# Performance work log

Measured on AMD Instinct MI355X. Metric: run time of the kernel, lower is better.

## Reference

```python
import jax, jax.numpy as jnp
import numpy as np

B, S, D = 4, 2048, 1024
E = 8            # num_experts
F = 4096         # expert hidden dim (4*D)
T = B * S        # tokens
CAP = 1280       # capacity = ceil(1.25 * T / E)


def setup_inputs() -> dict:
    key = jax.random.key(0)
    k1, k2, k3, k4 = jax.random.split(key, 4)
    inputs = jax.random.normal(k1, (B, S, D), dtype=jnp.float32)
    gate_w = jax.random.normal(k2, (D, E), dtype=jnp.float32) / np.sqrt(D)
    w1 = jax.random.normal(k3, (E, D, F), dtype=jnp.float32) / np.sqrt(D)
    w2 = jax.random.normal(k4, (E, F, D), dtype=jnp.float32) / np.sqrt(F)
    return {"inputs": inputs, "gate_w": gate_w, "w1": w1, "w2": w2}


def reference(inputs, gate_w, w1, w2):
    tokens = inputs.reshape(-1, D)                       # [T, D]
    logits = tokens @ gate_w                             # [T, E] (gate, no bias)
    probs = jax.nn.softmax(logits, axis=-1)
    expert_idx = jnp.argmax(probs, axis=-1)              # top-1 routing
    mask1 = jax.nn.one_hot(expert_idx, E, dtype=tokens.dtype)        # [T, E]
    # position of each token within its chosen expert's queue
    pos = (jnp.cumsum(mask1, axis=0) - 1.0).astype(jnp.int32)        # [T, E]
    # one_hot of out-of-range (>= CAP) positions is all-zero -> capacity drop
    sec_mask = mask1[:, :, None] * jax.nn.one_hot(pos, CAP, dtype=tokens.dtype)  # [T, E, C]
    combine_weights = probs[:, :, None] * sec_mask       # [T, E, C]
    # dispatch: matmul(sec_mask.permute(1,2,0), tokens) -> [E, C, D]
    expert_input = jnp.einsum('tec,td->ecd', sec_mask, tokens)
    # grouped per-expert FFN
    h = jax.nn.relu(jnp.einsum('ecd,edf->ecf', expert_input, w1))    # [E, C, F]
    expert_output = jnp.einsum('ecf,efd->ecd', h, w2)                # [E, C, D]
    # combine: [T, E*C] @ [E*C, D]
    out = jnp.einsum('tec,ecd->td', combine_weights, expert_output)  # [T, D]
    return out.reshape(inputs.shape)
```

## Files before the change

### kernel.cpp

```cpp
#include <hip/hip_runtime.h>
#include <hip/hip_bf16.h>

#define TOKENS   8192
#define DDIM     1024
#define NEXP     8
#define FDIM     4096
#define CAPACITY 1280
#define NYT      10

typedef __attribute__((ext_vector_type(8))) __bf16 bf16x8;
typedef __attribute__((ext_vector_type(4))) __bf16 bf16x4;
typedef __attribute__((ext_vector_type(4))) float  f32x4;

typedef __attribute__((address_space(1))) const void gvoid_t;
typedef __attribute__((address_space(3))) void       lvoid_t;

__device__ __forceinline__ void async16(const void* g, void* l) {
  __builtin_amdgcn_global_load_lds((gvoid_t*)g, (lvoid_t*)l, 16, 0, 0);
}

__global__ void gate_kernel(const float* __restrict__ x, const float* __restrict__ gw,
                            int* __restrict__ eidx, float* __restrict__ prob) {
  const int t = blockIdx.x;
  const int lane = threadIdx.x;
  const float* xp = x + (size_t)t * DDIM;
  float acc[NEXP];
#pragma unroll
  for (int e = 0; e < NEXP; ++e) acc[e] = 0.f;
#pragma unroll 4
  for (int i = 0; i < DDIM / 64; ++i) {
    const int d = i * 64 + lane;
    const float xv = xp[d];
    const f32x4 g0 = *(const f32x4*)(gw + d * NEXP);
    const f32x4 g1 = *(const f32x4*)(gw + d * NEXP + 4);
    acc[0] += xv * g0[0]; acc[1] += xv * g0[1];
    acc[2] += xv * g0[2]; acc[3] += xv * g0[3];
    acc[4] += xv * g1[0]; acc[5] += xv * g1[1];
    acc[6] += xv * g1[2]; acc[7] += xv * g1[3];
  }
#pragma unroll
  for (int e = 0; e < NEXP; ++e) {
    float v = acc[e];
#pragma unroll
    for (int off = 32; off; off >>= 1) v += __shfl_xor(v, off);
    acc[e] = v;
  }
  if (lane == 0) {
    float m = acc[0]; int mi = 0;
#pragma unroll
    for (int e = 1; e < NEXP; ++e) if (acc[e] > m) { m = acc[e]; mi = e; }
    float s = 0.f;
#pragma unroll
    for (int e = 0; e < NEXP; ++e) s += __expf(acc[e] - m);
    eidx[t] = mi;
    prob[t] = 1.f / s;
  }
}

__global__ void scan_kernel(const int* __restrict__ eidx, int* __restrict__ src,
                            int* __restrict__ counts) {
  __shared__ int buf[2][NEXP][256];
  const int tid = threadIdx.x;
  for (int i = tid; i < NEXP * CAPACITY; i += 256) src[i] = -1;
  const int t0 = tid * (TOKENS / 256);
#pragma unroll
  for (int e = 0; e < NEXP; ++e) buf[0][e][tid] = 0;
  for (int k = 0; k < TOKENS / 256; ++k) {
    const int e = eidx[t0 + k];
    buf[0][e][tid]++;
  }
  __syncthreads();
  int cur = 0;
  for (int off = 1; off < 256; off <<= 1) {
#pragma unroll
    for (int e = 0; e < NEXP; ++e) {
      int v = buf[cur][e][tid];
      if (tid >= off) v += buf[cur][e][tid - off];
      buf[cur ^ 1][e][tid] = v;
    }
    __syncthreads();
    cur ^= 1;
  }
  if (tid < NEXP) counts[tid] = buf[cur][tid][255];
#pragma unroll
  for (int e = 0; e < NEXP; ++e)
    buf[cur ^ 1][e][tid] = (tid > 0) ? buf[cur][e][tid - 1] : 0;
  for (int k = 0; k < TOKENS / 256; ++k) {
    const int t = t0 + k;
    const int e = eidx[t];
    const int p = buf[cur ^ 1][e][tid]++;
    if (p < CAPACITY) src[e * CAPACITY + p] = t;
  }
}

__global__ void dispatch_kernel(const float* __restrict__ tokens, const int* __restrict__ src,
                                __bf16* __restrict__ Xb) {
  const int slot = blockIdx.x;
  const int tid  = threadIdx.x;
  const int t = src[slot];
  bf16x4* dst = (bf16x4*)(Xb + (size_t)slot * DDIM);
  bf16x4 o;
  if (t >= 0) {
    const f32x4 v = ((const f32x4*)(tokens + (size_t)t * DDIM))[tid];
    o[0] = (__bf16)v[0]; o[1] = (__bf16)v[1]; o[2] = (__bf16)v[2]; o[3] = (__bf16)v[3];
  } else {
    o[0] = (__bf16)0.f; o[1] = (__bf16)0.f; o[2] = (__bf16)0.f; o[3] = (__bf16)0.f;
  }
  dst[tid] = o;
}

__global__ void transpose_convert_kernel(const float* __restrict__ w, __bf16* __restrict__ wt,
                                         int R, int C) {
  __shared__ __bf16 tile[64][65];
  const int e = blockIdx.z;
  const float* wp = w + (size_t)e * R * C;
  __bf16* op = wt + (size_t)e * R * C;
  const int c0 = blockIdx.x * 64, r0 = blockIdx.y * 64;
  const int tx = threadIdx.x, ty = threadIdx.y;
#pragma unroll
  for (int i = 0; i < 16; ++i) {
    const int r = ty + i * 4;
    tile[r][tx] = (__bf16)wp[(size_t)(r0 + r) * C + c0 + tx];
  }
  __syncthreads();
#pragma unroll
  for (int i = 0; i < 16; ++i) {
    const int cc = ty + i * 4;
    op[(size_t)(c0 + cc) * R + r0 + tx] = tile[tx][cc];
  }
}

template <int MODE>
__global__ __launch_bounds__(256, 2)
void gemm_kernel(const __bf16* __restrict__ A, const __bf16* __restrict__ B,
                 __bf16* __restrict__ Cbf, float* __restrict__ out,
                 const int* __restrict__ src, const float* __restrict__ prob,
                 const int* __restrict__ counts,
                 int K, size_t sA, size_t sB, size_t sC) {
  constexpr int N  = (MODE == 0) ? FDIM : DDIM;
  constexpr int NX = N / 128;
  __shared__ char lds[2][32768];

  const int nwg = NX * NYT * NEXP;
  int wg = blockIdx.x;
  wg = (wg & 7) * (nwg >> 3) + (wg >> 3);
  const int e   = wg / (NX * NYT);
  const int rem = wg - e * (NX * NYT);
  const int ty  = rem % NYT;
  const int tx  = rem / NYT;
  const int m0  = ty * 128, n0 = tx * 128;

  const int cnt   = counts[e];
  const int tiles = (cnt + 127) >> 7;
  if (ty >= ((tiles < NYT) ? tiles : NYT)) return;

  const __bf16* Ae = A + (size_t)e * sA;
  const __bf16* Be = B + (size_t)e * sB;
  const int tid = threadIdx.x;
  const int wid = tid >> 6, lane = tid & 63;
  const int wm = wid >> 1, wn = wid & 1;
  const int rl = lane & 15, gl = lane >> 4;
  const int wu = __builtin_amdgcn_readfirstlane(tid) >> 6;

  f32x4 acc[4][4];
#pragma unroll
  for (int m = 0; m < 4; ++m)
#pragma unroll
    for (int n = 0; n < 4; ++n) acc[m][n] = (f32x4){0.f, 0.f, 0.f, 0.f};

  auto stage = [&](int c, int kt) {
    const int k0 = kt * 64;
#pragma unroll
    for (int i = 0; i < 4; ++i) {
      const int chunk = i * 4 + wu;
      const int s = chunk * 64 + lane;
      const int row = s >> 3, cg = (s & 7) ^ (row & 7);
      async16(Ae + (size_t)(m0 + row) * K + k0 + cg * 8, &lds[c][chunk * 1024]);
      async16(Be + (size_t)(n0 + row) * K + k0 + cg * 8, &lds[c][16384 + chunk * 1024]);
    }
  };

  auto phase = [&](int c, int kk) {
    bf16x8 af[4], bv[4];
#pragma unroll
    for (int m = 0; m < 4; ++m) {
      const int rowin = wm * 64 + m * 16 + rl;
      af[m] = *(const bf16x8*)(&lds[c][rowin * 128 + (((kk * 4 + gl) ^ (rowin & 7)) * 16)]);
    }
#pragma unroll
    for (int n = 0; n < 4; ++n) {
      const int rowin = wn * 64 + n * 16 + rl;
      bv[n] = *(const bf16x8*)(&lds[c][16384 + rowin * 128 +
                                       (((kk * 4 + gl) ^ (rowin & 7)) * 16)]);
    }
    __builtin_amdgcn_s_setprio(1);
#pragma unroll
    for (int m = 0; m < 4; ++m)
#pragma unroll
      for (int n = 0; n < 4; ++n)
        acc[m][n] = __builtin_amdgcn_mfma_f32_16x16x32_bf16(af[m], bv[n], acc[m][n], 0, 0, 0);
    __builtin_amdgcn_s_setprio(0);
  };

  const int nkt = K >> 6;
  stage(0, 0);
  __syncthreads();
  for (int t = 0; t < nkt; ++t) {
    const int cur = t & 1;
    if (t + 1 < nkt) stage(cur ^ 1, t + 1);
    phase(cur, 0);
    phase(cur, 1);
    if (t + 1 < nkt) __syncthreads();
  }

  if (MODE == 0) {
    __bf16* Ce = Cbf + (size_t)e * sC;
#pragma unroll
    for (int m = 0; m < 4; ++m)
#pragma unroll
      for (int j = 0; j < 4; ++j) {
        const int row = m0 + wm * 64 + m * 16 + gl * 4 + j;
#pragma unroll
        for (int n = 0; n < 4; ++n) {
          const int col = n0 + wn * 64 + n * 16 + rl;
          float v = acc[m][n][j];
          v = v > 0.f ? v : 0.f;
          Ce[(size_t)row * N + col] = (__bf16)v;
        }
      }
  } else {
#pragma unroll
    for (int m = 0; m < 4; ++m)
#pragma unroll
      for (int j = 0; j < 4; ++j) {
        const int slot = m0 + wm * 64 + m * 16 + gl * 4 + j;
        const int t = src[e * CAPACITY + slot];
        if (t >= 0) {
          const float p = prob[t];
          float* op = out + (size_t)t * N;
#pragma unroll
          for (int n = 0; n < 4; ++n) {
            const int col = n0 + wn * 64 + n * 16 + rl;
            op[col] = p * acc[m][n][j];
          }
        }
      }
  }
}

extern "C" void kernel_launch(void* const* d_in, const int* in_sizes, int n_in,
                              void* d_out, int out_size, void* d_ws, size_t ws_size,
                              hipStream_t stream) {
  const float* x  = (const float*)d_in[0];
  const float* gw = (const float*)d_in[1];
  const float* w1 = (const float*)d_in[2];
  const float* w2 = (const float*)d_in[3];
  float* out = (float*)d_out;

  char* ws = (char*)d_ws;
  size_t off = 0;
  auto alloc = [&](size_t bytes) {
    void* p = ws + off;
    off += (bytes + 255) & ~(size_t)255;
    return p;
  };
  __bf16* W1bT = (__bf16*)alloc((size_t)NEXP * FDIM * DDIM * 2);
  __bf16* W2bT = (__bf16*)alloc((size_t)NEXP * DDIM * FDIM * 2);
  __bf16* Xb   = (__bf16*)alloc((size_t)NEXP * CAPACITY * DDIM * 2);
  __bf16* Hb   = (__bf16*)alloc((size_t)NEXP * CAPACITY * FDIM * 2);
  int*   eidx  = (int*)alloc(TOKENS * sizeof(int));
  float* prob  = (float*)alloc(TOKENS * sizeof(float));
  int*   srcm  = (int*)alloc(NEXP * CAPACITY * sizeof(int));
  int*   cnts  = (int*)alloc(NEXP * sizeof(int));
  (void)ws_size; (void)in_sizes; (void)n_in;

  hipMemsetAsync(d_out, 0, (size_t)out_size * sizeof(float), stream);

  gate_kernel<<<TOKENS, 64, 0, stream>>>(x, gw, eidx, prob);
  scan_kernel<<<1, 256, 0, stream>>>(eidx, srcm, cnts);
  dispatch_kernel<<<NEXP * CAPACITY, 256, 0, stream>>>(x, srcm, Xb);
  transpose_convert_kernel<<<dim3(FDIM / 64, DDIM / 64, NEXP), dim3(64, 4), 0, stream>>>(
      w1, W1bT, DDIM, FDIM);
  transpose_convert_kernel<<<dim3(DDIM / 64, FDIM / 64, NEXP), dim3(64, 4), 0, stream>>>(
      w2, W2bT, FDIM, DDIM);
  gemm_kernel<0><<<(FDIM / 128) * NYT * NEXP, 256, 0, stream>>>(
      Xb, W1bT, Hb, nullptr, nullptr, nullptr, cnts,
      DDIM, (size_t)CAPACITY * DDIM, (size_t)FDIM * DDIM, (size_t)CAPACITY * FDIM);
  gemm_kernel<1><<<(DDIM / 128) * NYT * NEXP, 256, 0, stream>>>(
      Hb, W2bT, nullptr, out, srcm, prob, cnts,
      FDIM, (size_t)CAPACITY * FDIM, (size_t)DDIM * FDIM, 0);
}
```

Measured before the change: 366.9 us.

## Vectorize weight transpose and single-buffer the grouped GEMM LDS staging

The weight transpose-convert kernel now reads float4 vectors and writes 8-wide bf16 vectors through a padded tile, cutting scalar global memory transactions. The GEMM drops its double-buffered async prefetch and s_setprio hints in favour of a simple load, sync, compute, sync loop with half the LDS. The smaller LDS footprint may allow more resident workgroups, but global loads no longer overlap with MFMA work inside a workgroup.

```diff
diff --git a/kernel.cpp b/kernel.cpp
--- a/kernel.cpp
+++ b/kernel.cpp
@@ -111,22 +111,29 @@
 
 __global__ void transpose_convert_kernel(const float* __restrict__ w, __bf16* __restrict__ wt,
                                          int R, int C) {
-  __shared__ __bf16 tile[64][65];
+  __shared__ __bf16 tile[64][66];
   const int e = blockIdx.z;
   const float* wp = w + (size_t)e * R * C;
   __bf16* op = wt + (size_t)e * R * C;
   const int c0 = blockIdx.x * 64, r0 = blockIdx.y * 64;
-  const int tx = threadIdx.x, ty = threadIdx.y;
-#pragma unroll
-  for (int i = 0; i < 16; ++i) {
-    const int r = ty + i * 4;
-    tile[r][tx] = (__bf16)wp[(size_t)(r0 + r) * C + c0 + tx];
+  const int tid = threadIdx.x;
+#pragma unroll
+  for (int p = 0; p < 4; ++p) {
+    const int r = p * 16 + (tid >> 4);
+    const int c = (tid & 15) * 4;
+    const f32x4 v = *(const f32x4*)(wp + (size_t)(r0 + r) * C + c0 + c);
+    tile[r][c]     = (__bf16)v[0]; tile[r][c + 1] = (__bf16)v[1];
+    tile[r][c + 2] = (__bf16)v[2]; tile[r][c + 3] = (__bf16)v[3];
   }
   __syncthreads();
 #pragma unroll
-  for (int i = 0; i < 16; ++i) {
-    const int cc = ty + i * 4;
-    op[(size_t)(c0 + cc) * R + r0 + tx] = tile[tx][cc];
+  for (int p = 0; p < 2; ++p) {
+    const int c  = p * 32 + (tid >> 3);
+    const int rg = (tid & 7) * 8;
+    bf16x8 o;
+#pragma unroll
+    for (int i = 0; i < 8; ++i) o[i] = tile[rg + i][c];
+    *(bf16x8*)(op + (size_t)(c0 + c) * R + r0 + rg) = o;
   }
 }
 
@@ -139,7 +146,7 @@
                  int K, size_t sA, size_t sB, size_t sC) {
   constexpr int N  = (MODE == 0) ? FDIM : DDIM;
   constexpr int NX = N / 128;
-  __shared__ char lds[2][32768];
+  __shared__ __bf16 lds[2][128 * 64];
 
   const int nwg = NX * NYT * NEXP;
   int wg = blockIdx.x;
@@ -160,7 +167,6 @@
   const int wid = tid >> 6, lane = tid & 63;
   const int wm = wid >> 1, wn = wid & 1;
   const int rl = lane & 15, gl = lane >> 4;
-  const int wu = __builtin_amdgcn_readfirstlane(tid) >> 6;
 
   f32x4 acc[4][4];
 #pragma unroll
@@ -168,49 +174,38 @@
 #pragma unroll
     for (int n = 0; n < 4; ++n) acc[m][n] = (f32x4){0.f, 0.f, 0.f, 0.f};
 
-  auto stage = [&](int c, int kt) {
-    const int k0 = kt * 64;
+  for (int kt = 0; kt < K; kt += 64) {
 #pragma unroll
     for (int i = 0; i < 4; ++i) {
-      const int chunk = i * 4 + wu;
-      const int s = chunk * 64 + lane;
-      const int row = s >> 3, cg = (s & 7) ^ (row & 7);
-      async16(Ae + (size_t)(m0 + row) * K + k0 + cg * 8, &lds[c][chunk * 1024]);
-      async16(Be + (size_t)(n0 + row) * K + k0 + cg * 8, &lds[c][16384 + chunk * 1024]);
+      const int s   = (wid * 4 + i) * 64 + lane;
+      const int row = s >> 3;
+      const int cg  = (s & 7) ^ (row & 7);
+      async16(Ae + (size_t)(m0 + row) * K + kt + cg * 8, &lds[0][(wid * 4 + i) * 512]);
+      async16(Be + (size_t)(n0 + row) * K + kt + cg * 8, &lds[1][(wid * 4 + i) * 512]);
     }
-  };
-
-  auto phase = [&](int c, int kk) {
-    bf16x8 af[4], bv[4];
-#pragma unroll
-    for (int m = 0; m < 4; ++m) {
-      const int rowin = wm * 64 + m * 16 + rl;
-      af[m] = *(const bf16x8*)(&lds[c][rowin * 128 + (((kk * 4 + gl) ^ (rowin & 7)) * 16)]);
+    __syncthreads();
+    const char* la = (const char*)&lds[0][0];
+    const char* lb = (const char*)&lds[1][0];
+#pragma unroll
+    for (int kk = 0; kk < 2; ++kk) {
+      bf16x8 af[4], bv[4];
+#pragma unroll
+      for (int m = 0; m < 4; ++m) {
+        const int rowin = wm * 64 + m * 16 + rl;
+        af[m] = *(const bf16x8*)(la + rowin * 128 + (((kk * 4 + gl) ^ (rowin & 7)) * 16));
+      }
+#pragma unroll
+      for (int n = 0; n < 4; ++n) {
+        const int rowin = wn * 64 + n * 16 + rl;
+        bv[n] = *(const bf16x8*)(lb + rowin * 128 + (((kk * 4 + gl) ^ (rowin & 7)) * 16));
+      }
+#pragma unroll
+      for (int m = 0; m < 4; ++m)
+#pragma unroll
+        for (int n = 0; n < 4; ++n)
+          acc[m][n] = __builtin_amdgcn_mfma_f32_16x16x32_bf16(af[m], bv[n], acc[m][n], 0, 0, 0);
     }
-#pragma unroll
-    for (int n = 0; n < 4; ++n) {
-      const int rowin = wn * 64 + n * 16 + rl;
-      bv[n] = *(const bf16x8*)(&lds[c][16384 + rowin * 128 +
-                                       (((kk * 4 + gl) ^ (rowin & 7)) * 16)]);
-    }
-    __builtin_amdgcn_s_setprio(1);
-#pragma unroll
-    for (int m = 0; m < 4; ++m)
-#pragma unroll
-      for (int n = 0; n < 4; ++n)
-        acc[m][n] = __builtin_amdgcn_mfma_f32_16x16x32_bf16(af[m], bv[n], acc[m][n], 0, 0, 0);
-    __builtin_amdgcn_s_setprio(0);
-  };
-
-  const int nkt = K >> 6;
-  stage(0, 0);
-  __syncthreads();
-  for (int t = 0; t < nkt; ++t) {
-    const int cur = t & 1;
-    if (t + 1 < nkt) stage(cur ^ 1, t + 1);
-    phase(cur, 0);
-    phase(cur, 1);
-    if (t + 1 < nkt) __syncthreads();
+    __syncthreads();
   }
 
   if (MODE == 0) {
@@ -279,9 +274,9 @@
   gate_kernel<<<TOKENS, 64, 0, stream>>>(x, gw, eidx, prob);
   scan_kernel<<<1, 256, 0, stream>>>(eidx, srcm, cnts);
   dispatch_kernel<<<NEXP * CAPACITY, 256, 0, stream>>>(x, srcm, Xb);
-  transpose_convert_kernel<<<dim3(FDIM / 64, DDIM / 64, NEXP), dim3(64, 4), 0, stream>>>(
+  transpose_convert_kernel<<<dim3(FDIM / 64, DDIM / 64, NEXP), 256, 0, stream>>>(
       w1, W1bT, DDIM, FDIM);
-  transpose_convert_kernel<<<dim3(DDIM / 64, FDIM / 64, NEXP), dim3(64, 4), 0, stream>>>(
+  transpose_convert_kernel<<<dim3(DDIM / 64, FDIM / 64, NEXP), 256, 0, stream>>>(
       w2, W2bT, FDIM, DDIM);
   gemm_kernel<0><<<(FDIM / 128) * NYT * NEXP, 256, 0, stream>>>(
       Xb, W1bT, Hb, nullptr, nullptr, nullptr, cnts,
```

New measurement: 326.5 us. 11.0% less time.
